# Kernel optimization log

Measured on AMD Instinct MI355X. Metric: run time of the kernel, lower is better.

## Reference

```python
import jax, jax.numpy as jnp
import numpy as np

B, D = 8192, 2048
H1, H2, G = 1024, 512, 512
T, SPEC, SH = 2, 2, 2
E = T * SPEC + SH          # total experts = 6
EC = SPEC + SH             # experts per task = 4


def setup_inputs() -> dict:
    key = jax.random.key(0)
    ks = jax.random.split(key, 6)
    s = 0.02  # glorot-ish scale
    return {
        "x":   jax.random.normal(ks[0], (B, D), jnp.float32),
        "We1": jax.random.normal(ks[1], (E, D, H1), jnp.float32) * s,
        "be1": jnp.zeros((E, H1), jnp.float32),
        "We2": jax.random.normal(ks[2], (E, H1, H2), jnp.float32) * s,
        "be2": jnp.zeros((E, H2), jnp.float32),
        "Wg1": jax.random.normal(ks[3], (T, D, G), jnp.float32) * s,
        "bg1": jnp.zeros((T, G), jnp.float32),
        "Wgs": jax.random.normal(ks[4], (T, G, EC), jnp.float32) * s,
    }


# per-task expert indices: task i uses its SPEC specific experts + the SH shared (last) experts
_IDX = np.array([[i * SPEC + j for j in range(SPEC)] + list(range(T * SPEC, E))
                 for i in range(T)])  # [T, EC]


def reference(x, We1, be1, We2, be2, Wg1, bg1, Wgs):
    # All experts batched into grouped GEMMs (the fusion the original loop misses)
    h1 = jax.nn.relu(jnp.einsum('bd,edh->beh', x, We1) + be1)        # [B,E,H1]
    h2 = jax.nn.relu(jnp.einsum('beh,eho->beo', h1, We2) + be2)      # [B,E,H2]
    # Gate MLP per task, batched over tasks
    g = jax.nn.relu(jnp.einsum('bd,tdg->btg', x, Wg1) + bg1)         # [B,T,G]
    gate = jax.nn.softmax(jnp.einsum('btg,tge->bte', g, Wgs), axis=-1)  # [B,T,EC]
    sel = h2[:, _IDX, :]                                             # [B,T,EC,H2]
    out = jnp.einsum('bteo,bte->tbo', sel, gate)                     # [T,B,H2]
    return out
```

## Files before the change

### kernel.cpp

```cpp
#include <hip/hip_runtime.h>
#include <hip/hip_bf16.h>
#include <cstdint>
#include <cstddef>

#define B_   8192
#define D_   2048
#define H1_  1024
#define H2_  512
#define G_   512
#define T_   2
#define E_   6
#define EC_  4

typedef __bf16 bf16_t;
typedef __attribute__((ext_vector_type(8))) __bf16 bf16x8;
typedef __attribute__((ext_vector_type(4))) float f32x4;

__device__ __forceinline__ void gload_lds16(const bf16_t* g, bf16_t* l) {
    __builtin_amdgcn_global_load_lds(
        (const __attribute__((address_space(1))) bf16_t*)g,
        (__attribute__((address_space(3))) bf16_t*)l,
        16, 0, 0);
}

__global__ __launch_bounds__(256) void cast_x_kernel(
    const float* __restrict__ src, bf16_t* __restrict__ dst, int n8)
{
    int i = blockIdx.x * blockDim.x + threadIdx.x;
    if (i >= n8) return;
    const float4* s = (const float4*)src + (size_t)i * 2;
    float4 a = s[0], b = s[1];
    bf16x8 o;
    o[0] = (bf16_t)a.x; o[1] = (bf16_t)a.y; o[2] = (bf16_t)a.z; o[3] = (bf16_t)a.w;
    o[4] = (bf16_t)b.x; o[5] = (bf16_t)b.y; o[6] = (bf16_t)b.z; o[7] = (bf16_t)b.w;
    *(bf16x8*)(dst + (size_t)i * 8) = o;
}

__global__ __launch_bounds__(256) void transpose_cast_kernel(
    const float* __restrict__ src, bf16_t* __restrict__ dst, int R, int C)
{
    __shared__ float tile[32][33];
    int bz = blockIdx.z;
    src += (size_t)bz * R * C;
    dst += (size_t)bz * R * C;
    int c0 = blockIdx.x * 32, r0 = blockIdx.y * 32;
    int tx = threadIdx.x, ty = threadIdx.y;
#pragma unroll
    for (int i = 0; i < 32; i += 8)
        tile[ty + i][tx] = src[(size_t)(r0 + ty + i) * C + (c0 + tx)];
    __syncthreads();
#pragma unroll
    for (int i = 0; i < 32; i += 8)
        dst[(size_t)(c0 + ty + i) * R + (r0 + tx)] = (bf16_t)tile[tx][ty + i];
}

__global__ __launch_bounds__(512, 4) void gemm_bn256_bias_relu(
    const bf16_t* __restrict__ A, const bf16_t* __restrict__ Bt,
    const float* __restrict__ bias, bf16_t* __restrict__ C,
    int M, int N, int K, long long strideA)
{
    const int e = blockIdx.z;
    A    += (size_t)e * (size_t)strideA;
    Bt   += (size_t)e * (size_t)N * (size_t)K;
    bias += (size_t)e * (size_t)N;
    C    += (size_t)e * (size_t)M * (size_t)N;

    const int gx  = gridDim.x;
    const int nwg = gx * gridDim.y;
    const int lin = blockIdx.y * gx + blockIdx.x;
    const int swz = (lin & 7) * (nwg >> 3) + (lin >> 3);
    const int row0 = (swz / gx) * 128;
    const int col0 = (swz % gx) * 256;

    __shared__ bf16_t lsA[3][128 * 32];
    __shared__ bf16_t lsB[3][256 * 32];

    const int tid  = threadIdx.x;
    const int lane = tid & 63;
    const int wave = tid >> 6;
    const int wr   = wave >> 2;
    const int wc   = wave & 3;

    size_t offA, offB0, offB1;
    {
        int rA = tid >> 2, pA = tid & 3;
        offA = (size_t)rA * (size_t)K + (size_t)(((pA ^ (rA >> 1)) & 3) * 8);
        int r0_ = tid >> 2, p0_ = tid & 3;
        offB0 = (size_t)r0_ * (size_t)K + (size_t)(((p0_ ^ (r0_ >> 1)) & 3) * 8);
        int r1_ = (512 + tid) >> 2, p1_ = tid & 3;
        offB1 = (size_t)r1_ * (size_t)K + (size_t)(((p1_ ^ (r1_ >> 1)) & 3) * 8);
    }
    const int ldsA_off = wave * 512;
    const int ldsB0off = wave * 512;
    const int ldsB1off = 4096 + wave * 512;

    const bf16_t* gA = A  + (size_t)row0 * (size_t)K;
    const bf16_t* gB = Bt + (size_t)col0 * (size_t)K;

    const int xch  = ((lane >> 4) ^ ((lane >> 1) & 3)) << 3;
    const int aoff = (wr * 64 + (lane & 15)) * 32 + xch;
    const int boff = (wc * 64 + (lane & 15)) * 32 + xch;

    f32x4 acc[4][4];
#pragma unroll
    for (int m = 0; m < 4; ++m)
#pragma unroll
        for (int n = 0; n < 4; ++n)
            acc[m][n] = (f32x4){0.f, 0.f, 0.f, 0.f};

    const int nt = K >> 5;

#define STAGE(t_, c_) do {                                                    \
    const size_t kk_ = (size_t)(t_) * 32;                                     \
    gload_lds16(gA + kk_ + offA,  &lsA[c_][ldsA_off]);                        \
    gload_lds16(gB + kk_ + offB0, &lsB[c_][ldsB0off]);                        \
    gload_lds16(gB + kk_ + offB1, &lsB[c_][ldsB1off]);                        \
} while (0)

    STAGE(0, 0); STAGE(1, 1); STAGE(2, 2);
    asm volatile("s_waitcnt vmcnt(6)" ::: "memory");
    __builtin_amdgcn_s_barrier();
    __builtin_amdgcn_sched_barrier(0);

    int c = 0;
    for (int t = 0; t < nt; ++t) {
        bf16x8 a[4], b[4];
#pragma unroll
        for (int m = 0; m < 4; ++m)
            a[m] = *(const bf16x8*)&lsA[c][aoff + m * 512];
#pragma unroll
        for (int n = 0; n < 4; ++n)
            b[n] = *(const bf16x8*)&lsB[c][boff + n * 512];
        asm volatile("s_waitcnt lgkmcnt(0)" ::: "memory");
        __builtin_amdgcn_sched_barrier(0);
        __builtin_amdgcn_s_barrier();
        __builtin_amdgcn_sched_barrier(0);
        if (t + 3 < nt) STAGE(t + 3, c);
        __builtin_amdgcn_sched_barrier(0);
        __builtin_amdgcn_s_setprio(1);
#pragma unroll
        for (int m = 0; m < 4; ++m)
#pragma unroll
            for (int n = 0; n < 4; ++n)
                acc[m][n] = __builtin_amdgcn_mfma_f32_16x16x32_bf16(
                                a[m], b[n], acc[m][n], 0, 0, 0);
        __builtin_amdgcn_s_setprio(0);
        __builtin_amdgcn_sched_barrier(0);
        if (t + 3 < nt) { asm volatile("s_waitcnt vmcnt(6)" ::: "memory"); }
        else            { asm volatile("s_waitcnt vmcnt(0)" ::: "memory"); }
        __builtin_amdgcn_sched_barrier(0);
        __builtin_amdgcn_s_barrier();
        __builtin_amdgcn_sched_barrier(0);
        c = (c == 2) ? 0 : c + 1;
    }
#undef STAGE

    const int crb = row0 + wr * 64 + ((lane >> 4) << 2);
    const int ccb = col0 + wc * 64 + (lane & 15);
#pragma unroll
    for (int n = 0; n < 4; ++n) {
        const int cc = ccb + n * 16;
        const float bv = bias[cc];
#pragma unroll
        for (int m = 0; m < 4; ++m) {
            const int rb = crb + m * 16;
#pragma unroll
            for (int j = 0; j < 4; ++j) {
                float v = acc[m][n][j] + bv;
                v = v > 0.f ? v : 0.f;
                C[(size_t)(rb + j) * N + cc] = (bf16_t)v;
            }
        }
    }
}

__global__ __launch_bounds__(256) void gate_kernel(
    const bf16_t* __restrict__ h1, const float* __restrict__ Wgs,
    float* __restrict__ gate)
{
    int wid  = blockIdx.x * 4 + (threadIdx.x >> 6);
    int lane = threadIdx.x & 63;
    int t = wid >> 13;
    int b = wid & (B_ - 1);
    const bf16_t* grow = h1 + ((size_t)(6 * B_) + b) * 1024 + t * G_;
    bf16x8 gv = *(const bf16x8*)&grow[lane * 8];
    const float* W = Wgs + (size_t)t * G_ * EC_;
    float a0 = 0.f, a1 = 0.f, a2 = 0.f, a3 = 0.f;
#pragma unroll
    for (int i = 0; i < 8; ++i) {
        float gvf = (float)gv[i];
        const float4 w = *(const float4*)&W[(size_t)(lane * 8 + i) * 4];
        a0 += gvf * w.x; a1 += gvf * w.y; a2 += gvf * w.z; a3 += gvf * w.w;
    }
#pragma unroll
    for (int off = 32; off; off >>= 1) {
        a0 += __shfl_xor(a0, off);
        a1 += __shfl_xor(a1, off);
        a2 += __shfl_xor(a2, off);
        a3 += __shfl_xor(a3, off);
    }
    if (lane == 0) {
        float m  = fmaxf(fmaxf(a0, a1), fmaxf(a2, a3));
        float e0 = expf(a0 - m), e1 = expf(a1 - m), e2 = expf(a2 - m), e3 = expf(a3 - m);
        float inv = 1.f / (e0 + e1 + e2 + e3);
        *(float4*)&gate[(size_t)wid * 4] = make_float4(e0 * inv, e1 * inv, e2 * inv, e3 * inv);
    }
}

__global__ __launch_bounds__(256) void combine_kernel(
    const bf16_t* __restrict__ h2, const float* __restrict__ gate,
    float* __restrict__ out)
{
    size_t idx = (size_t)blockIdx.x * 256 + threadIdx.x;
    size_t tb  = idx >> 6;
    int    o0  = (int)(idx & 63) * 8;
    int    t   = (int)(tb >> 13);
    size_t b   = tb & (size_t)(B_ - 1);
    const float4 gv = *(const float4*)&gate[tb * 4];
    const bf16x8 v0 = *(const bf16x8*)&h2[((size_t)(2 * t)     * B_ + b) * H2_ + o0];
    const bf16x8 v1 = *(const bf16x8*)&h2[((size_t)(2 * t + 1) * B_ + b) * H2_ + o0];
    const bf16x8 v2 = *(const bf16x8*)&h2[((size_t)4           * B_ + b) * H2_ + o0];
    const bf16x8 v3 = *(const bf16x8*)&h2[((size_t)5           * B_ + b) * H2_ + o0];
    float r[8];
#pragma unroll
    for (int i = 0; i < 8; ++i)
        r[i] = gv.x * (float)v0[i] + gv.y * (float)v1[i]
             + gv.z * (float)v2[i] + gv.w * (float)v3[i];
    float4* op = (float4*)&out[tb * H2_ + o0];
    op[0] = make_float4(r[0], r[1], r[2], r[3]);
    op[1] = make_float4(r[4], r[5], r[6], r[7]);
}

extern "C" void kernel_launch(void* const* d_in, const int* in_sizes, int n_in,
                              void* d_out, int out_size, void* d_ws, size_t ws_size,
                              hipStream_t stream)
{
    const float* x   = (const float*)d_in[0];
    const float* We1 = (const float*)d_in[1];
    const float* be1 = (const float*)d_in[2];
    const float* We2 = (const float*)d_in[3];
    const float* be2 = (const float*)d_in[4];
    const float* Wg1 = (const float*)d_in[5];
    const float* bg1 = (const float*)d_in[6];
    const float* Wgs = (const float*)d_in[7];
    float* out = (float*)d_out;

    char* ws = (char*)d_ws;
    bf16_t* x_bf  = (bf16_t*)ws;  ws += (size_t)B_ * D_ * 2;
    bf16_t* w1t   = (bf16_t*)ws;  ws += (size_t)7 * H1_ * D_ * 2;
    bf16_t* w2t   = (bf16_t*)ws;  ws += (size_t)E_ * H2_ * H1_ * 2;
    bf16_t* h1    = (bf16_t*)ws;  ws += (size_t)7 * B_ * H1_ * 2;
    bf16_t* h2    = (bf16_t*)ws;  ws += (size_t)E_ * B_ * H2_ * 2;
    float*  bias7 = (float*)ws;   ws += (size_t)7 * H1_ * 4;
    float*  gate  = (float*)ws;   ws += (size_t)T_ * B_ * EC_ * 4;

    bf16_t* wgt = w1t + (size_t)6 * H1_ * D_;

    hipMemcpyAsync(bias7, be1, (size_t)E_ * H1_ * sizeof(float),
                   hipMemcpyDeviceToDevice, stream);
    hipMemcpyAsync(bias7 + (size_t)E_ * H1_, bg1, (size_t)T_ * G_ * sizeof(float),
                   hipMemcpyDeviceToDevice, stream);

    cast_x_kernel<<<(B_ * D_ / 8) / 256, 256, 0, stream>>>(x, x_bf, B_ * D_ / 8);
    dim3 tb(32, 8);
    transpose_cast_kernel<<<dim3(H1_ / 32, D_ / 32, E_),  tb, 0, stream>>>(We1, w1t, D_,  H1_);
    transpose_cast_kernel<<<dim3(H2_ / 32, H1_ / 32, E_), tb, 0, stream>>>(We2, w2t, H1_, H2_);
    transpose_cast_kernel<<<dim3(G_ / 32, D_ / 32, T_),   tb, 0, stream>>>(Wg1, wgt, D_,  G_);

    gemm_bn256_bias_relu<<<dim3(H1_ / 256, B_ / 128, 7), 512, 0, stream>>>(
        x_bf, w1t, bias7, h1, B_, H1_, D_, 0LL);
    gemm_bn256_bias_relu<<<dim3(H2_ / 256, B_ / 128, E_), 512, 0, stream>>>(
        h1, w2t, be2, h2, B_, H2_, H1_, (long long)B_ * H1_);

    gate_kernel<<<(T_ * B_) / 4, 256, 0, stream>>>(h1, Wgs, gate);
    combine_kernel<<<((size_t)T_ * B_ * H2_ / 8) / 256, 256, 0, stream>>>(h2, gate, out);
}
```

Before: 381.7 us.

## Enlarge GEMM tile to 256x256 with 4-stage pipeline and register double-buffering

Turns the grouped GEMM into a kernel templated on K and doubles the M tile from 128 to 256 rows, so each wave computes a 128x64 sub-tile with 32 accumulators. It moves to a 4-deep LDS ring buffer with a fully unrolled steady state, where the register fragments for the next k-step are read from LDS while the current MFMAs run. The aim is more arithmetic per byte loaded, fewer barriers per FLOP and better overlap of LDS reads with MFMA. The cost is much higher register and LDS use, so occupancy drops to 2 blocks per CU and the grid has half as many workgroups.

```diff
diff --git a/kernel.cpp b/kernel.cpp
--- a/kernel.cpp
+++ b/kernel.cpp
@@ -54,11 +54,16 @@
         dst[(size_t)(c0 + ty + i) * R + (r0 + tx)] = (bf16_t)tile[tx][ty + i];
 }
 
-__global__ __launch_bounds__(512, 4) void gemm_bn256_bias_relu(
+template<int K>
+__global__ __launch_bounds__(512, 2) void gemm256_tpl(
     const bf16_t* __restrict__ A, const bf16_t* __restrict__ Bt,
     const float* __restrict__ bias, bf16_t* __restrict__ C,
-    int M, int N, int K, long long strideA)
-{
+    int M, int N, long long strideA)
+{
+    constexpr int NT   = K / 32;
+    constexpr int MAIN = NT - 4;
+    static_assert(K % 128 == 0, "NT must be multiple of 4");
+
     const int e = blockIdx.z;
     A    += (size_t)e * (size_t)strideA;
     Bt   += (size_t)e * (size_t)N * (size_t)K;
@@ -69,11 +74,11 @@
     const int nwg = gx * gridDim.y;
     const int lin = blockIdx.y * gx + blockIdx.x;
     const int swz = (lin & 7) * (nwg >> 3) + (lin >> 3);
-    const int row0 = (swz / gx) * 128;
+    const int row0 = (swz / gx) * 256;
     const int col0 = (swz % gx) * 256;
 
-    __shared__ bf16_t lsA[3][128 * 32];
-    __shared__ bf16_t lsB[3][256 * 32];
+    __shared__ bf16_t lsA[4][8192];
+    __shared__ bf16_t lsB[4][8192];
 
     const int tid  = threadIdx.x;
     const int lane = tid & 63;
@@ -81,88 +86,107 @@
     const int wr   = wave >> 2;
     const int wc   = wave & 3;
 
-    size_t offA, offB0, offB1;
-    {
-        int rA = tid >> 2, pA = tid & 3;
-        offA = (size_t)rA * (size_t)K + (size_t)(((pA ^ (rA >> 1)) & 3) * 8);
-        int r0_ = tid >> 2, p0_ = tid & 3;
-        offB0 = (size_t)r0_ * (size_t)K + (size_t)(((p0_ ^ (r0_ >> 1)) & 3) * 8);
-        int r1_ = (512 + tid) >> 2, p1_ = tid & 3;
-        offB1 = (size_t)r1_ * (size_t)K + (size_t)(((p1_ ^ (r1_ >> 1)) & 3) * 8);
-    }
-    const int ldsA_off = wave * 512;
-    const int ldsB0off = wave * 512;
-    const int ldsB1off = 4096 + wave * 512;
-
-    const bf16_t* gA = A  + (size_t)row0 * (size_t)K;
-    const bf16_t* gB = Bt + (size_t)col0 * (size_t)K;
+    size_t offs[2];
+#pragma unroll
+    for (int l = 0; l < 2; ++l) {
+        int idx = l * 512 + tid;
+        int r   = idx >> 2;
+        int c   = (idx & 3) ^ ((r >> 1) & 3);
+        offs[l] = (size_t)r * (size_t)K + (size_t)(c * 8);
+    }
+    const int ldsOff0 = wave * 512;
+    const int ldsOff1 = 4096 + wave * 512;
+
+    const bf16_t* pA0 = A  + (size_t)row0 * (size_t)K + offs[0];
+    const bf16_t* pA1 = A  + (size_t)row0 * (size_t)K + offs[1];
+    const bf16_t* pB0 = Bt + (size_t)col0 * (size_t)K + offs[0];
+    const bf16_t* pB1 = Bt + (size_t)col0 * (size_t)K + offs[1];
 
     const int xch  = ((lane >> 4) ^ ((lane >> 1) & 3)) << 3;
-    const int aoff = (wr * 64 + (lane & 15)) * 32 + xch;
-    const int boff = (wc * 64 + (lane & 15)) * 32 + xch;
-
-    f32x4 acc[4][4];
-#pragma unroll
-    for (int m = 0; m < 4; ++m)
+    const int aoff = (wr * 128 + (lane & 15)) * 32 + xch;
+    const int boff = (wc * 64  + (lane & 15)) * 32 + xch;
+
+    f32x4 acc[8][4];
+#pragma unroll
+    for (int m = 0; m < 8; ++m)
 #pragma unroll
         for (int n = 0; n < 4; ++n)
             acc[m][n] = (f32x4){0.f, 0.f, 0.f, 0.f};
 
-    const int nt = K >> 5;
-
-#define STAGE(t_, c_) do {                                                    \
-    const size_t kk_ = (size_t)(t_) * 32;                                     \
-    gload_lds16(gA + kk_ + offA,  &lsA[c_][ldsA_off]);                        \
-    gload_lds16(gB + kk_ + offB0, &lsB[c_][ldsB0off]);                        \
-    gload_lds16(gB + kk_ + offB1, &lsB[c_][ldsB1off]);                        \
+    bf16x8 aF0[8], bF0[4], aF1[8], bF1[4];
+
+#define STAGE(kt_, bi_) do {                                                  \
+    gload_lds16(pA0 + (size_t)(kt_) * 32, &lsA[bi_][ldsOff0]);                \
+    gload_lds16(pA1 + (size_t)(kt_) * 32, &lsA[bi_][ldsOff1]);                \
+    gload_lds16(pB0 + (size_t)(kt_) * 32, &lsB[bi_][ldsOff0]);                \
+    gload_lds16(pB1 + (size_t)(kt_) * 32, &lsB[bi_][ldsOff1]);                \
 } while (0)
 
-    STAGE(0, 0); STAGE(1, 1); STAGE(2, 2);
-    asm volatile("s_waitcnt vmcnt(6)" ::: "memory");
+#define RD(nx_, bi_) do {                                                     \
+    _Pragma("unroll")                                                         \
+    for (int m_ = 0; m_ < 8; ++m_)                                            \
+        aF##nx_[m_] = *(const bf16x8*)&lsA[bi_][aoff + m_ * 512];             \
+    _Pragma("unroll")                                                         \
+    for (int n_ = 0; n_ < 4; ++n_)                                            \
+        bF##nx_[n_] = *(const bf16x8*)&lsB[bi_][boff + n_ * 512];             \
+} while (0)
+
+#define MM(cu_) do {                                                          \
+    __builtin_amdgcn_s_setprio(1);                                            \
+    _Pragma("unroll")                                                         \
+    for (int m_ = 0; m_ < 8; ++m_)                                            \
+        _Pragma("unroll")                                                     \
+        for (int n_ = 0; n_ < 4; ++n_)                                        \
+            acc[m_][n_] = __builtin_amdgcn_mfma_f32_16x16x32_bf16(            \
+                aF##cu_[m_], bF##cu_[n_], acc[m_][n_], 0, 0, 0);              \
+    __builtin_amdgcn_s_setprio(0);                                            \
+} while (0)
+
+#define ENDI(vm_) do {                                                        \
+    asm volatile("s_waitcnt vmcnt(" #vm_ ") lgkmcnt(0)" ::: "memory");        \
+    __builtin_amdgcn_sched_barrier(0);                                        \
+    __builtin_amdgcn_s_barrier();                                             \
+    __builtin_amdgcn_sched_barrier(0);                                        \
+} while (0)
+
+    STAGE(0, 0); STAGE(1, 1); STAGE(2, 2); STAGE(3, 3);
+    asm volatile("s_waitcnt vmcnt(8)" ::: "memory");
+    __builtin_amdgcn_sched_barrier(0);
     __builtin_amdgcn_s_barrier();
     __builtin_amdgcn_sched_barrier(0);
-
-    int c = 0;
-    for (int t = 0; t < nt; ++t) {
-        bf16x8 a[4], b[4];
-#pragma unroll
-        for (int m = 0; m < 4; ++m)
-            a[m] = *(const bf16x8*)&lsA[c][aoff + m * 512];
-#pragma unroll
-        for (int n = 0; n < 4; ++n)
-            b[n] = *(const bf16x8*)&lsB[c][boff + n * 512];
-        asm volatile("s_waitcnt lgkmcnt(0)" ::: "memory");
-        __builtin_amdgcn_sched_barrier(0);
-        __builtin_amdgcn_s_barrier();
-        __builtin_amdgcn_sched_barrier(0);
-        if (t + 3 < nt) STAGE(t + 3, c);
-        __builtin_amdgcn_sched_barrier(0);
-        __builtin_amdgcn_s_setprio(1);
-#pragma unroll
-        for (int m = 0; m < 4; ++m)
-#pragma unroll
-            for (int n = 0; n < 4; ++n)
-                acc[m][n] = __builtin_amdgcn_mfma_f32_16x16x32_bf16(
-                                a[m], b[n], acc[m][n], 0, 0, 0);
-        __builtin_amdgcn_s_setprio(0);
-        __builtin_amdgcn_sched_barrier(0);
-        if (t + 3 < nt) { asm volatile("s_waitcnt vmcnt(6)" ::: "memory"); }
-        else            { asm volatile("s_waitcnt vmcnt(0)" ::: "memory"); }
-        __builtin_amdgcn_sched_barrier(0);
-        __builtin_amdgcn_s_barrier();
-        __builtin_amdgcn_sched_barrier(0);
-        c = (c == 2) ? 0 : c + 1;
-    }
+    RD(0, 0);
+    asm volatile("s_waitcnt lgkmcnt(0)" ::: "memory");
+    __builtin_amdgcn_sched_barrier(0);
+    __builtin_amdgcn_s_barrier();
+    __builtin_amdgcn_sched_barrier(0);
+
+    for (int tb = 0; tb < MAIN; tb += 4) {
+        STAGE(tb + 4, 0); RD(1, 1); MM(0); ENDI(8);
+        STAGE(tb + 5, 1); RD(0, 2); MM(1); ENDI(8);
+        STAGE(tb + 6, 2); RD(1, 3); MM(0); ENDI(8);
+        STAGE(tb + 7, 3); RD(0, 0); MM(1); ENDI(8);
+    }
+
+    RD(1, 1); MM(0); ENDI(4);
+    RD(0, 2); MM(1); ENDI(0);
+    RD(1, 3); MM(0);
+    asm volatile("s_waitcnt lgkmcnt(0)" ::: "memory");
+    __builtin_amdgcn_sched_barrier(0);
+    MM(1);
+
 #undef STAGE
-
-    const int crb = row0 + wr * 64 + ((lane >> 4) << 2);
-    const int ccb = col0 + wc * 64 + (lane & 15);
+#undef RD
+#undef MM
+#undef ENDI
+
+    const int crb = row0 + wr * 128 + ((lane >> 4) << 2);
+    const int ccb = col0 + wc * 64  + (lane & 15);
 #pragma unroll
     for (int n = 0; n < 4; ++n) {
         const int cc = ccb + n * 16;
         const float bv = bias[cc];
 #pragma unroll
-        for (int m = 0; m < 4; ++m) {
+        for (int m = 0; m < 8; ++m) {
             const int rb = crb + m * 16;
 #pragma unroll
             for (int j = 0; j < 4; ++j) {
@@ -267,10 +291,10 @@
     transpose_cast_kernel<<<dim3(H2_ / 32, H1_ / 32, E_), tb, 0, stream>>>(We2, w2t, H1_, H2_);
     transpose_cast_kernel<<<dim3(G_ / 32, D_ / 32, T_),   tb, 0, stream>>>(Wg1, wgt, D_,  G_);
 
-    gemm_bn256_bias_relu<<<dim3(H1_ / 256, B_ / 128, 7), 512, 0, stream>>>(
-        x_bf, w1t, bias7, h1, B_, H1_, D_, 0LL);
-    gemm_bn256_bias_relu<<<dim3(H2_ / 256, B_ / 128, E_), 512, 0, stream>>>(
-        h1, w2t, be2, h2, B_, H2_, H1_, (long long)B_ * H1_);
+    gemm256_tpl<2048><<<dim3(H1_ / 256, B_ / 256, 7), 512, 0, stream>>>(
+        x_bf, w1t, bias7, h1, B_, H1_, 0LL);
+    gemm256_tpl<1024><<<dim3(H2_ / 256, B_ / 256, E_), 512, 0, stream>>>(
+        h1, w2t, be2, h2, B_, H2_, (long long)B_ * H1_);
 
     gate_kernel<<<(T_ * B_) / 4, 256, 0, stream>>>(h1, Wgs, gate);
     combine_kernel<<<((size_t)T_ * B_ * H2_ / 8) / 256, 256, 0, stream>>>(h2, gate, out);
```

Measured after the change: 489.0 us. +28.1%, slower.

## Use 256x256 tile triple-buffered GEMM kernel for first layer

Applied to the files above, without the earlier changes.

Adds a new bf16 MFMA GEMM kernel with 256x256 output tiles, a three-stage LDS ring buffer fed by direct global-to-LDS loads, and swizzled LDS addressing. It replaces the 128x256 tile kernel for the first (largest) GEMM over the experts plus the gate layer. Larger tiles raise arithmetic intensity and cut redundant global loads of A and B, while the deeper pipeline hides memory latency. The cost is more accumulator registers and LDS (96 KB per block), which lowers occupancy to about two blocks per CU and risks register spills.

```diff
diff --git a/kernel.cpp b/kernel.cpp
--- a/kernel.cpp
+++ b/kernel.cpp
@@ -52,6 +52,127 @@
 #pragma unroll
     for (int i = 0; i < 32; i += 8)
         dst[(size_t)(c0 + ty + i) * R + (r0 + tx)] = (bf16_t)tile[tx][ty + i];
+}
+
+__global__ __launch_bounds__(512, 2) void gemm256_s_kernel(
+    const bf16_t* __restrict__ A, const bf16_t* __restrict__ Bt,
+    const float* __restrict__ bias, bf16_t* __restrict__ C,
+    int M, int N, int K, long long strideA)
+{
+    const int e = blockIdx.z;
+    A    += (size_t)e * (size_t)strideA;
+    Bt   += (size_t)e * (size_t)N * (size_t)K;
+    bias += (size_t)e * (size_t)N;
+    C    += (size_t)e * (size_t)M * (size_t)N;
+
+    const int gx  = gridDim.x;
+    const int nwg = gx * gridDim.y;
+    const int lin = blockIdx.y * gx + blockIdx.x;
+    const int swz = (lin & 7) * (nwg >> 3) + (lin >> 3);
+    const int row0 = (swz / gx) * 256;
+    const int col0 = (swz % gx) * 256;
+
+    __shared__ bf16_t lsA[3][8192];
+    __shared__ bf16_t lsB[3][8192];
+
+    const int tid  = threadIdx.x;
+    const int lane = tid & 63;
+    const int wave = tid >> 6;
+    const int wr   = wave >> 2;
+    const int wc   = wave & 3;
+
+    size_t offs[2];
+#pragma unroll
+    for (int l = 0; l < 2; ++l) {
+        int idx = l * 512 + tid;
+        int r   = idx >> 2;
+        int c   = (idx & 3) ^ ((r >> 1) & 3);
+        offs[l] = (size_t)r * (size_t)K + (size_t)(c * 8);
+    }
+    const int ldsOff0 = wave * 512;
+    const int ldsOff1 = 4096 + wave * 512;
+
+    const bf16_t* pA0 = A  + (size_t)row0 * (size_t)K + offs[0];
+    const bf16_t* pA1 = A  + (size_t)row0 * (size_t)K + offs[1];
+    const bf16_t* pB0 = Bt + (size_t)col0 * (size_t)K + offs[0];
+    const bf16_t* pB1 = Bt + (size_t)col0 * (size_t)K + offs[1];
+
+    const int xch  = ((lane >> 4) ^ ((lane >> 1) & 3)) << 3;
+    const int aoff = (wr * 128 + (lane & 15)) * 32 + xch;
+    const int boff = (wc * 64  + (lane & 15)) * 32 + xch;
+
+    f32x4 acc[8][4];
+#pragma unroll
+    for (int m = 0; m < 8; ++m)
+#pragma unroll
+        for (int n = 0; n < 4; ++n)
+            acc[m][n] = (f32x4){0.f, 0.f, 0.f, 0.f};
+
+    const int nt = K >> 5;
+
+#define STAGE(t_, c_) do {                                                    \
+    const size_t kk_ = (size_t)(t_) * 32;                                     \
+    gload_lds16(pA0 + kk_, &lsA[c_][ldsOff0]);                                \
+    gload_lds16(pA1 + kk_, &lsA[c_][ldsOff1]);                                \
+    gload_lds16(pB0 + kk_, &lsB[c_][ldsOff0]);                                \
+    gload_lds16(pB1 + kk_, &lsB[c_][ldsOff1]);                                \
+} while (0)
+
+    STAGE(0, 0); STAGE(1, 1); STAGE(2, 2);
+    asm volatile("s_waitcnt vmcnt(8)" ::: "memory");
+    __builtin_amdgcn_s_barrier();
+    __builtin_amdgcn_sched_barrier(0);
+
+    int c = 0;
+    for (int t = 0; t < nt; ++t) {
+        bf16x8 a[8], b[4];
+#pragma unroll
+        for (int m = 0; m < 8; ++m)
+            a[m] = *(const bf16x8*)&lsA[c][aoff + m * 512];
+#pragma unroll
+        for (int n = 0; n < 4; ++n)
+            b[n] = *(const bf16x8*)&lsB[c][boff + n * 512];
+        asm volatile("s_waitcnt lgkmcnt(0)" ::: "memory");
+        __builtin_amdgcn_sched_barrier(0);
+        __builtin_amdgcn_s_barrier();
+        __builtin_amdgcn_sched_barrier(0);
+        if (t + 3 < nt) STAGE(t + 3, c);
+        __builtin_amdgcn_sched_barrier(0);
+        __builtin_amdgcn_s_setprio(1);
+#pragma unroll
+        for (int m = 0; m < 8; ++m)
+#pragma unroll
+            for (int n = 0; n < 4; ++n)
+                acc[m][n] = __builtin_amdgcn_mfma_f32_16x16x32_bf16(
+                                a[m], b[n], acc[m][n], 0, 0, 0);
+        __builtin_amdgcn_s_setprio(0);
+        __builtin_amdgcn_sched_barrier(0);
+        if (t + 3 < nt) { asm volatile("s_waitcnt vmcnt(8)" ::: "memory"); }
+        else            { asm volatile("s_waitcnt vmcnt(0)" ::: "memory"); }
+        __builtin_amdgcn_sched_barrier(0);
+        __builtin_amdgcn_s_barrier();
+        __builtin_amdgcn_sched_barrier(0);
+        c = (c == 2) ? 0 : c + 1;
+    }
+#undef STAGE
+
+    const int crb = row0 + wr * 128 + ((lane >> 4) << 2);
+    const int ccb = col0 + wc * 64  + (lane & 15);
+#pragma unroll
+    for (int n = 0; n < 4; ++n) {
+        const int cc = ccb + n * 16;
+        const float bv = bias[cc];
+#pragma unroll
+        for (int m = 0; m < 8; ++m) {
+            const int rb = crb + m * 16;
+#pragma unroll
+            for (int j = 0; j < 4; ++j) {
+                float v = acc[m][n][j] + bv;
+                v = v > 0.f ? v : 0.f;
+                C[(size_t)(rb + j) * N + cc] = (bf16_t)v;
+            }
+        }
+    }
 }
 
 __global__ __launch_bounds__(512, 4) void gemm_bn256_bias_relu(
@@ -267,7 +388,7 @@
     transpose_cast_kernel<<<dim3(H2_ / 32, H1_ / 32, E_), tb, 0, stream>>>(We2, w2t, H1_, H2_);
     transpose_cast_kernel<<<dim3(G_ / 32, D_ / 32, T_),   tb, 0, stream>>>(Wg1, wgt, D_,  G_);
 
-    gemm_bn256_bias_relu<<<dim3(H1_ / 256, B_ / 128, 7), 512, 0, stream>>>(
+    gemm256_s_kernel<<<dim3(H1_ / 256, B_ / 256, 7), 512, 0, stream>>>(
         x_bf, w1t, bias7, h1, B_, H1_, D_, 0LL);
     gemm_bn256_bias_relu<<<dim3(H2_ / 256, B_ / 128, E_), 512, 0, stream>>>(
         h1, w2t, be2, h2, B_, H2_, H1_, (long long)B_ * H1_);
```

Result: slower. 426.1 us (+11.6%).

## Load GEMM A operand directly from global into registers, bypassing LDS

Applied to the files above, without the earlier changes.

Removes the LDS staging buffer for the A tile in the grouped bias+ReLU GEMM. Each wave now loads its A fragments straight from global memory into registers, one K-step ahead, while B keeps its triple-buffered global-to-LDS pipeline. This cuts LDS traffic and footprint. In exchange, the four column-waves sharing a row block each fetch the same A rows, so A global loads are duplicated. Because the A loads are issued after the MFMAs and consumed in the next iteration, their latency is poorly hidden, and the in-order vmcnt wait for them may also drain the B prefetch queue.

```diff
diff --git a/kernel.cpp b/kernel.cpp
--- a/kernel.cpp
+++ b/kernel.cpp
@@ -54,7 +54,7 @@
         dst[(size_t)(c0 + ty + i) * R + (r0 + tx)] = (bf16_t)tile[tx][ty + i];
 }
 
-__global__ __launch_bounds__(512, 4) void gemm_bn256_bias_relu(
+__global__ __launch_bounds__(512, 4) void gemm_adirect(
     const bf16_t* __restrict__ A, const bf16_t* __restrict__ Bt,
     const float* __restrict__ bias, bf16_t* __restrict__ C,
     int M, int N, int K, long long strideA)
@@ -72,8 +72,7 @@
     const int row0 = (swz / gx) * 128;
     const int col0 = (swz % gx) * 256;
 
-    __shared__ bf16_t lsA[3][128 * 32];
-    __shared__ bf16_t lsB[3][256 * 32];
+    __shared__ bf16_t lsB[3][8192];
 
     const int tid  = threadIdx.x;
     const int lane = tid & 63;
@@ -81,25 +80,26 @@
     const int wr   = wave >> 2;
     const int wc   = wave & 3;
 
-    size_t offA, offB0, offB1;
+    size_t offB0, offB1;
     {
-        int rA = tid >> 2, pA = tid & 3;
-        offA = (size_t)rA * (size_t)K + (size_t)(((pA ^ (rA >> 1)) & 3) * 8);
         int r0_ = tid >> 2, p0_ = tid & 3;
         offB0 = (size_t)r0_ * (size_t)K + (size_t)(((p0_ ^ (r0_ >> 1)) & 3) * 8);
         int r1_ = (512 + tid) >> 2, p1_ = tid & 3;
         offB1 = (size_t)r1_ * (size_t)K + (size_t)(((p1_ ^ (r1_ >> 1)) & 3) * 8);
     }
-    const int ldsA_off = wave * 512;
     const int ldsB0off = wave * 512;
     const int ldsB1off = 4096 + wave * 512;
-
-    const bf16_t* gA = A  + (size_t)row0 * (size_t)K;
     const bf16_t* gB = Bt + (size_t)col0 * (size_t)K;
 
     const int xch  = ((lane >> 4) ^ ((lane >> 1) & 3)) << 3;
-    const int aoff = (wr * 64 + (lane & 15)) * 32 + xch;
     const int boff = (wc * 64 + (lane & 15)) * 32 + xch;
+
+    const bf16_t* pa = A + (size_t)(row0 + wr * 64 + (lane & 15)) * (size_t)K
+                         + ((lane >> 4) << 3);
+    const bf16_t* pa0 = pa;
+    const bf16_t* pa1 = pa + (size_t)16 * (size_t)K;
+    const bf16_t* pa2 = pa + (size_t)32 * (size_t)K;
+    const bf16_t* pa3 = pa + (size_t)48 * (size_t)K;
 
     f32x4 acc[4][4];
 #pragma unroll
@@ -110,24 +110,24 @@
 
     const int nt = K >> 5;
 
-#define STAGE(t_, c_) do {                                                    \
+#define STAGEB(t_, c_) do {                                                   \
     const size_t kk_ = (size_t)(t_) * 32;                                     \
-    gload_lds16(gA + kk_ + offA,  &lsA[c_][ldsA_off]);                        \
     gload_lds16(gB + kk_ + offB0, &lsB[c_][ldsB0off]);                        \
     gload_lds16(gB + kk_ + offB1, &lsB[c_][ldsB1off]);                        \
 } while (0)
 
-    STAGE(0, 0); STAGE(1, 1); STAGE(2, 2);
-    asm volatile("s_waitcnt vmcnt(6)" ::: "memory");
+    STAGEB(0, 0); STAGEB(1, 1); STAGEB(2, 2);
+    bf16x8 a0 = *(const bf16x8*)pa0;
+    bf16x8 a1 = *(const bf16x8*)pa1;
+    bf16x8 a2 = *(const bf16x8*)pa2;
+    bf16x8 a3 = *(const bf16x8*)pa3;
+    asm volatile("s_waitcnt vmcnt(0)" ::: "memory");
     __builtin_amdgcn_s_barrier();
     __builtin_amdgcn_sched_barrier(0);
 
     int c = 0;
     for (int t = 0; t < nt; ++t) {
-        bf16x8 a[4], b[4];
-#pragma unroll
-        for (int m = 0; m < 4; ++m)
-            a[m] = *(const bf16x8*)&lsA[c][aoff + m * 512];
+        bf16x8 b[4];
 #pragma unroll
         for (int n = 0; n < 4; ++n)
             b[n] = *(const bf16x8*)&lsB[c][boff + n * 512];
@@ -135,25 +135,31 @@
         __builtin_amdgcn_sched_barrier(0);
         __builtin_amdgcn_s_barrier();
         __builtin_amdgcn_sched_barrier(0);
-        if (t + 3 < nt) STAGE(t + 3, c);
+        if (t + 3 < nt) STAGEB(t + 3, c);
         __builtin_amdgcn_sched_barrier(0);
         __builtin_amdgcn_s_setprio(1);
 #pragma unroll
-        for (int m = 0; m < 4; ++m)
-#pragma unroll
-            for (int n = 0; n < 4; ++n)
-                acc[m][n] = __builtin_amdgcn_mfma_f32_16x16x32_bf16(
-                                a[m], b[n], acc[m][n], 0, 0, 0);
+        for (int n = 0; n < 4; ++n) {
+            acc[0][n] = __builtin_amdgcn_mfma_f32_16x16x32_bf16(a0, b[n], acc[0][n], 0, 0, 0);
+            acc[1][n] = __builtin_amdgcn_mfma_f32_16x16x32_bf16(a1, b[n], acc[1][n], 0, 0, 0);
+            acc[2][n] = __builtin_amdgcn_mfma_f32_16x16x32_bf16(a2, b[n], acc[2][n], 0, 0, 0);
+            acc[3][n] = __builtin_amdgcn_mfma_f32_16x16x32_bf16(a3, b[n], acc[3][n], 0, 0, 0);
+        }
         __builtin_amdgcn_s_setprio(0);
         __builtin_amdgcn_sched_barrier(0);
-        if (t + 3 < nt) { asm volatile("s_waitcnt vmcnt(6)" ::: "memory"); }
-        else            { asm volatile("s_waitcnt vmcnt(0)" ::: "memory"); }
+        if (t + 1 < nt) {
+            const size_t ko = (size_t)(t + 1) * 32;
+            a0 = *(const bf16x8*)(pa0 + ko);
+            a1 = *(const bf16x8*)(pa1 + ko);
+            a2 = *(const bf16x8*)(pa2 + ko);
+            a3 = *(const bf16x8*)(pa3 + ko);
+        }
         __builtin_amdgcn_sched_barrier(0);
         __builtin_amdgcn_s_barrier();
         __builtin_amdgcn_sched_barrier(0);
         c = (c == 2) ? 0 : c + 1;
     }
-#undef STAGE
+#undef STAGEB
 
     const int crb = row0 + wr * 64 + ((lane >> 4) << 2);
     const int ccb = col0 + wc * 64 + (lane & 15);
@@ -267,9 +273,9 @@
     transpose_cast_kernel<<<dim3(H2_ / 32, H1_ / 32, E_), tb, 0, stream>>>(We2, w2t, H1_, H2_);
     transpose_cast_kernel<<<dim3(G_ / 32, D_ / 32, T_),   tb, 0, stream>>>(Wg1, wgt, D_,  G_);
 
-    gemm_bn256_bias_relu<<<dim3(H1_ / 256, B_ / 128, 7), 512, 0, stream>>>(
+    gemm_adirect<<<dim3(H1_ / 256, B_ / 128, 7), 512, 0, stream>>>(
         x_bf, w1t, bias7, h1, B_, H1_, D_, 0LL);
-    gemm_bn256_bias_relu<<<dim3(H2_ / 256, B_ / 128, E_), 512, 0, stream>>>(
+    gemm_adirect<<<dim3(H2_ / 256, B_ / 128, E_), 512, 0, stream>>>(
         h1, w2t, be2, h2, B_, H2_, H1_, (long long)B_ * H1_);
 
     gate_kernel<<<(T_ * B_) / 4, 256, 0, stream>>>(h1, Wgs, gate);
```

After: 681.9 us. 78.6% more time.
